# Optimization experiments

Hardware: AMD Instinct MI355X
Metric: run time of the kernel (lower is better)

Reference implementation:

```python
import jax, jax.numpy as jnp
import numpy as np
from jax import lax

K = 3      # kernel_size
STRIDE = 1
PAD = 1
N_BASIS = 8


def _cheb_basis(x, n):
    # Chebyshev basis T_k(tanh(x)), k = 1..n  -> (..., n)
    t = jnp.arccos(jnp.tanh(x))
    ks = jnp.arange(1, n + 1, dtype=x.dtype)
    return jnp.cos(t[..., None] * ks)


def setup_inputs() -> dict:
    key = jax.random.key(0)
    k1, k2, k3 = jax.random.split(key, 3)
    b, cin, h, w = 16, 16, 64, 64
    cout = 32
    x = jax.random.normal(k1, (b, cin, h, w), dtype=jnp.float32)
    # params as in __init__: normal_(w), normal_(c, 0, 0.001)
    w_p = jax.random.normal(k2, (cin, cout, K * K, 1), dtype=jnp.float32)
    c_p = jax.random.normal(k3, (cin, cout, K * K, 1, N_BASIS), dtype=jnp.float32) * 0.001
    return {"x": x, "w": w_p, "c": c_p}


def reference(x, w, c):
    b, cin, h, wd = x.shape
    ho = (h - K + 2 * PAD) // STRIDE + 1
    wo = (wd - K + 2 * PAD) // STRIDE + 1
    L = ho * wo
    # unfold: (b, cin*K*K, ho, wo), channel-major like F.unfold
    patches = lax.conv_general_dilated_patches(
        x, (K, K), (STRIDE, STRIDE), [(PAD, PAD), (PAD, PAD)])
    wx = patches.reshape(b, cin, K * K, L)            # (b,i,k,l)
    res = jax.nn.silu(wx)                              # residual activation
    basis = _cheb_basis(wx, N_BASIS)                   # (b,i,k,l,n)
    w_sq = w[..., 0]                                   # (i,o,k)
    c_sq = c[:, :, :, 0, :]                            # (i,o,k,n)
    # sum_{i,k} w[i,o,k] * (res[b,i,k,l] + sum_n c[i,o,k,n]*basis[b,i,k,l,n])
    out = (jnp.einsum('iok,bikl->bol', w_sq, res)
           + jnp.einsum('iokn,bikln->bol', w_sq[..., None] * c_sq, basis))
    return out.reshape(b, -1, ho, wo)
```

## Files before the change

kernel.cpp:

```cpp
#include <hip/hip_runtime.h>

#define CIN 16
#define COUT 32
#define NB 8
#define HW 4096
#define PPW 66
#define KF 160
#define NCH 20
#define FROWS 6
#define PLANE 397

typedef short bf16x8 __attribute__((ext_vector_type(8)));
typedef float f32x4 __attribute__((ext_vector_type(4)));

__device__ inline unsigned short f2bf(float f) {
    unsigned u = __builtin_bit_cast(unsigned, f);
    u += 0x7FFFu + ((u >> 16) & 1u);
    return (unsigned short)(u >> 16);
}
__device__ inline unsigned pk(float a, float b) {
    return (unsigned)f2bf(a) | ((unsigned)f2bf(b) << 16);
}

#define WF_N (9 * COUT * KF)
#define LDS_BYTES (NCH * PLANE * 16)

__global__ __launch_bounds__(512) void kan_wf(const float* __restrict__ w,
                                              const float* __restrict__ c,
                                              unsigned short* __restrict__ wfl) {
    const int t = blockIdx.x * 512 + threadIdx.x;
    const int e    = t & 7;
    const int lane = (t >> 3) & 63;
    const int frag = t >> 9;
    const int shift = frag / 10;
    const int r     = frag % 10;
    const int st    = r >> 1;
    const int f     = r & 1;
    const int o     = f * 16 + (lane & 15);
    const int kel   = st * 32 + (lane >> 4) * 8 + e;
    const int i     = kel / 10, n = kel % 10;
    float val = 0.f;
    if (n != 9) {
        const float wv = w[(size_t)(i * COUT + o) * 9 + shift];
        val = (n == 0) ? wv : wv * c[((size_t)(i * COUT + o) * 9 + shift) * NB + (n - 1)];
    }
    wfl[t] = f2bf(val);
}

__global__ __launch_bounds__(1024, 4) void kan_main(const float* __restrict__ x,
                                                    const unsigned short* __restrict__ wfl,
                                                    float* __restrict__ out) {
    extern __shared__ __align__(16) unsigned short lds[];

    const int bid = blockIdx.x;
    const int b   = bid >> 4;
    const int y0  = (bid & 15) * 4;
    const int tid = threadIdx.x;

    for (int item = tid; item < 4 * FROWS * PPW; item += 1024) {
        const int cg  = item / (FROWS * PPW);
        const int rem = item - cg * (FROWS * PPW);
        const int lr  = rem / PPW;
        const int px  = rem - lr * PPW;
        const int iy  = y0 + lr - 1;

        unsigned rw[20];
        const bool valid = (iy >= 0) & (iy < 64) & (px >= 1) & (px <= 64);
        if (valid) {
            const int ix = px - 1;
#pragma unroll
            for (int j = 0; j < 4; ++j) {
                const int i = cg * 4 + j;
                const float v  = x[((size_t)(b * CIN + i)) * HW + iy * 64 + ix];
                const float p  = __expf(-v);
                const float p2 = p * p;
                const float s  = v * __builtin_amdgcn_rcpf(1.f + p);
                const float u  = (1.f - p2) * __builtin_amdgcn_rcpf(1.f + p2);
                const float u2 = 2.f * u;
                const float t1 = u;
                const float t2 = u2 * u - 1.f;
                const float t3 = u2 * t2 - t1;
                const float t4 = u2 * t3 - t2;
                const float t5 = u2 * t4 - t3;
                const float t6 = u2 * t5 - t4;
                const float t7 = u2 * t6 - t5;
                const float t8 = u2 * t7 - t6;
                rw[j * 5 + 0] = pk(s, t1);
                rw[j * 5 + 1] = pk(t2, t3);
                rw[j * 5 + 2] = pk(t4, t5);
                rw[j * 5 + 3] = pk(t6, t7);
                rw[j * 5 + 4] = (unsigned)f2bf(t8);
            }
        } else {
#pragma unroll
            for (int j = 0; j < 20; ++j) rw[j] = 0u;
        }
        const int base = lr * PPW + px;
#pragma unroll
        for (int q = 0; q < 5; ++q)
            *(uint4*)&lds[((cg * 5 + q) * PLANE + base) * 8] =
                make_uint4(rw[4 * q], rw[4 * q + 1], rw[4 * q + 2], rw[4 * q + 3]);
    }

    __syncthreads();

    const int l   = tid & 63;
    const int wv  = tid >> 6;
    const int ry  = wv >> 2;
    const int x0  = (wv & 3) * 16;
    const int col = l & 15;
    const int quad = l >> 4;

    const unsigned short* abase = wfl + l * 8;

    f32x4 acc0 = {0.f, 0.f, 0.f, 0.f};
    f32x4 acc1 = {0.f, 0.f, 0.f, 0.f};

#pragma unroll
    for (int shift = 0; shift < 9; ++shift) {
        const int dy = shift / 3 - 1, dx = shift % 3 - 1;
        const int base = (ry + 1 + dy) * PPW + (x0 + col + 1 + dx);
        const unsigned short* bb = lds + (quad * PLANE + base) * 8;
#pragma unroll
        for (int st = 0; st < 5; ++st) {
            const bf16x8 bf = *(const bf16x8*)(bb + (size_t)(st * 4) * PLANE * 8);
            const bf16x8 a0 = *(const bf16x8*)(abase + ((shift * 5 + st) * 2) * 512);
            const bf16x8 a1 = *(const bf16x8*)(abase + ((shift * 5 + st) * 2 + 1) * 512);
            acc0 = __builtin_amdgcn_mfma_f32_16x16x32_bf16(a0, bf, acc0, 0, 0, 0);
            acc1 = __builtin_amdgcn_mfma_f32_16x16x32_bf16(a1, bf, acc1, 0, 0, 0);
        }
    }

    float* op = out + (size_t)b * COUT * HW + (y0 + ry) * 64 + x0 + col;
#pragma unroll
    for (int r = 0; r < 4; ++r) {
        op[(size_t)(quad * 4 + r) * HW]      = acc0[r];
        op[(size_t)(quad * 4 + r + 16) * HW] = acc1[r];
    }
}

extern "C" void kernel_launch(void* const* d_in, const int* in_sizes, int n_in,
                              void* d_out, int out_size, void* d_ws, size_t ws_size,
                              hipStream_t stream) {
    const float* x = (const float*)d_in[0];
    const float* w = (const float*)d_in[1];
    const float* c = (const float*)d_in[2];
    float* out = (float*)d_out;

    unsigned short* wfl = (unsigned short*)d_ws;

    hipFuncSetAttribute((const void*)kan_main,
                        hipFuncAttributeMaxDynamicSharedMemorySize, LDS_BYTES);

    kan_wf<<<90, 512, 0, stream>>>(w, c, wfl);
    kan_main<<<256, 1024, LDS_BYTES, stream>>>(x, wfl, out);
}
```

Baseline: 25.52 us.

## Switch to 32x32x16 MFMA with K-split across wave pairs and LDS reduction

The kernel replaces the pair of 16x16x32 bf16 MFMAs per step with one 32x32x16 MFMA covering all 32 output channels and 32 pixels. The K dimension is split across two waves: each wave handles half the feature chunks, and the partial sums are combined through an added LDS reduction buffer. The weight-fragment layout kernel is rewritten to match the new operand layout. This halves the A-fragment loads per wave and uses the larger MFMA shape. In exchange it adds an extra barrier, extra LDS, and half of the waves sit idle during the store.

```diff
diff --git a/kernel.cpp b/kernel.cpp
--- a/kernel.cpp
+++ b/kernel.cpp
@@ -11,7 +11,7 @@
 #define PLANE 397
 
 typedef short bf16x8 __attribute__((ext_vector_type(8)));
-typedef float f32x4 __attribute__((ext_vector_type(4)));
+typedef float f32x16 __attribute__((ext_vector_type(16)));
 
 __device__ inline unsigned short f2bf(float f) {
     unsigned u = __builtin_bit_cast(unsigned, f);
@@ -22,8 +22,8 @@
     return (unsigned)f2bf(a) | ((unsigned)f2bf(b) << 16);
 }
 
-#define WF_N (9 * COUT * KF)
-#define LDS_BYTES (NCH * PLANE * 16)
+#define FEAT_SHORTS (NCH * PLANE * 8)
+#define LDS_BYTES (FEAT_SHORTS * 2 + 8 * 1024 * 4)
 
 __global__ __launch_bounds__(512) void kan_wf(const float* __restrict__ w,
                                               const float* __restrict__ c,
@@ -33,11 +33,9 @@
     const int lane = (t >> 3) & 63;
     const int frag = t >> 9;
     const int shift = frag / 10;
-    const int r     = frag % 10;
-    const int st    = r >> 1;
-    const int f     = r & 1;
-    const int o     = f * 16 + (lane & 15);
-    const int kel   = st * 32 + (lane >> 4) * 8 + e;
+    const int st    = frag % 10;
+    const int o     = lane & 31;
+    const int kel   = st * 16 + (lane >> 5) * 8 + e;
     const int i     = kel / 10, n = kel % 10;
     float val = 0.f;
     if (n != 9) {
@@ -104,38 +102,49 @@
 
     __syncthreads();
 
-    const int l   = tid & 63;
-    const int wv  = tid >> 6;
-    const int ry  = wv >> 2;
-    const int x0  = (wv & 3) * 16;
-    const int col = l & 15;
-    const int quad = l >> 4;
+    const int l    = tid & 63;
+    const int wv   = tid >> 6;
+    const int pg   = wv >> 1;
+    const int par  = wv & 1;
+    const int ry   = pg >> 1;
+    const int x0   = (pg & 1) * 32;
+    const int colp = l & 31;
+    const int hi   = l >> 5;
 
     const unsigned short* abase = wfl + l * 8;
 
-    f32x4 acc0 = {0.f, 0.f, 0.f, 0.f};
-    f32x4 acc1 = {0.f, 0.f, 0.f, 0.f};
+    f32x16 acc;
+#pragma unroll
+    for (int r = 0; r < 16; ++r) acc[r] = 0.f;
 
 #pragma unroll
     for (int shift = 0; shift < 9; ++shift) {
         const int dy = shift / 3 - 1, dx = shift % 3 - 1;
-        const int base = (ry + 1 + dy) * PPW + (x0 + col + 1 + dx);
-        const unsigned short* bb = lds + (quad * PLANE + base) * 8;
+        const int base = (ry + 1 + dy) * PPW + (x0 + colp + 1 + dx);
+        const unsigned short* aq = abase + (shift * 10 + par) * 512;
+        const unsigned short* bb = lds + ((2 * par + hi) * PLANE + base) * 8;
 #pragma unroll
-        for (int st = 0; st < 5; ++st) {
-            const bf16x8 bf = *(const bf16x8*)(bb + (size_t)(st * 4) * PLANE * 8);
-            const bf16x8 a0 = *(const bf16x8*)(abase + ((shift * 5 + st) * 2) * 512);
-            const bf16x8 a1 = *(const bf16x8*)(abase + ((shift * 5 + st) * 2 + 1) * 512);
-            acc0 = __builtin_amdgcn_mfma_f32_16x16x32_bf16(a0, bf, acc0, 0, 0, 0);
-            acc1 = __builtin_amdgcn_mfma_f32_16x16x32_bf16(a1, bf, acc1, 0, 0, 0);
+        for (int t = 0; t < 5; ++t) {
+            const bf16x8 bf = *(const bf16x8*)(bb + (size_t)(4 * t) * PLANE * 8);
+            const bf16x8 av = *(const bf16x8*)(aq + (2 * t) * 512);
+            acc = __builtin_amdgcn_mfma_f32_32x32x16_bf16(av, bf, acc, 0, 0, 0);
         }
     }
 
-    float* op = out + (size_t)b * COUT * HW + (y0 + ry) * 64 + x0 + col;
+    float* red = (float*)(lds + FEAT_SHORTS);
+    if (par) {
 #pragma unroll
-    for (int r = 0; r < 4; ++r) {
-        op[(size_t)(quad * 4 + r) * HW]      = acc0[r];
-        op[(size_t)(quad * 4 + r + 16) * HW] = acc1[r];
+        for (int r = 0; r < 16; ++r) red[pg * 1024 + r * 64 + l] = acc[r];
+    }
+    __syncthreads();
+    if (!par) {
+        float* op = out + (size_t)b * COUT * HW + (y0 + ry) * 64 + x0 + colp;
+#pragma unroll
+        for (int r = 0; r < 16; ++r) {
+            const float v = acc[r] + red[pg * 1024 + r * 64 + l];
+            const int o = (r & 3) + 8 * (r >> 2) + 4 * hi;
+            op[(size_t)o * HW] = v;
+        }
     }
 }
 
```

Measured after the change: 21.29 us, median of 2. -16.6%, faster.
